# Kernel optimization log

Hardware: AMD Instinct MI355X
Metric: run time of the kernel (lower is better)

Reference implementation:

```python
import jax, jax.numpy as jnp
import numpy as np

SELECT_SIZE = 64
SM_SCALE = 0.07216878364870322  # 192 ** -0.5
V_HEAD_DIM = 128


def setup_inputs() -> dict:
    key = jax.random.key(0)
    k1, k2, k3, k4 = jax.random.split(key, 4)
    B, S, Hq, G, TOPK = 4, 2048, 16, 4, 16
    T = B * S
    NB = S // SELECT_SIZE  # 32 blocks per sequence
    q = jax.random.normal(k1, (T, Hq, 192), dtype=jnp.float32)
    k = jax.random.normal(k2, (T, Hq, 192), dtype=jnp.float32)
    v = jax.random.normal(k3, (T, Hq, V_HEAD_DIM), dtype=jnp.float32)
    idx = jax.random.randint(k4, (T, G, TOPK), 0, NB, dtype=jnp.int32)
    # guarantee block 0 is always selected so every causal row has >=1 valid key
    idx = idx.at[..., 0].set(0)
    idx = jnp.sort(idx, axis=-1)
    return {"q": q, "k": k, "v": v, "selected_indices": idx,
            "batch_size": B, "seq_len": S}


def reference(q, k, v, selected_indices, batch_size, seq_len):
    B, S = batch_size, seq_len
    Hq = q.shape[1]
    G = selected_indices.shape[1]
    Hg = Hq // G  # query heads per selection-score group
    nb = (S + SELECT_SIZE - 1) // SELECT_SIZE
    dv = v.shape[-1]

    # un-ragged: B equal-length sequences
    qg = q.reshape(B, S, G, Hg, -1)
    kg = k.reshape(B, S, G, Hg, -1)
    vg = v.reshape(B, S, G, Hg, -1)
    idx = selected_indices.reshape(B, S, G, -1)

    # which KV blocks are selected for each (query position, group): [B,S,G,nb]
    allowed_blk = (idx[..., None] == jnp.arange(nb, dtype=idx.dtype)).any(axis=-2)
    blk_of_pos = jnp.arange(S) // SELECT_SIZE
    pos_ok = allowed_blk[..., blk_of_pos]  # [B, Tq, G, Skv]
    causal = jnp.arange(S)[:, None] >= jnp.arange(S)[None, :]
    mask = pos_ok & causal[None, :, None, :]          # [B, Tq, G, Skv]
    mask = mask.transpose(0, 2, 1, 3)[:, :, None]      # [B, G, 1, Tq, Skv]

    scores = jnp.einsum('btghd,bsghd->bghts', qg, kg) * SM_SCALE
    scores = jnp.where(mask, scores, jnp.float32(-1e30))
    attn = jax.nn.softmax(scores, axis=-1)
    o = jnp.einsum('bghts,bsghd->btghd', attn, vg)
    return o.reshape(B * S, Hq * dv)
```

## Files before the change

### kernel.cpp

```cpp
#include <hip/hip_runtime.h>


typedef __attribute__((ext_vector_type(8))) _Float16 half8;
typedef __attribute__((ext_vector_type(4))) float f32x4;
typedef __attribute__((ext_vector_type(4))) unsigned int u32x4;

__device__ __forceinline__ half8 cvt8(const float4* p) {
  float4 a = p[0], b = p[1];
  half8 r;
  r[0] = (_Float16)a.x; r[1] = (_Float16)a.y; r[2] = (_Float16)a.z; r[3] = (_Float16)a.w;
  r[4] = (_Float16)b.x; r[5] = (_Float16)b.y; r[6] = (_Float16)b.z; r[7] = (_Float16)b.w;
  return r;
}

__device__ __forceinline__ half8 cvt8s(const float4* p, float s) {
  float4 a = p[0], b = p[1];
  half8 r;
  r[0] = (_Float16)(a.x * s); r[1] = (_Float16)(a.y * s);
  r[2] = (_Float16)(a.z * s); r[3] = (_Float16)(a.w * s);
  r[4] = (_Float16)(b.x * s); r[5] = (_Float16)(b.y * s);
  r[6] = (_Float16)(b.z * s); r[7] = (_Float16)(b.w * s);
  return r;
}

__device__ __forceinline__ void async16(const void* g, void* l) {
  __builtin_amdgcn_global_load_lds(
      (const __attribute__((address_space(1))) void*)g,
      (__attribute__((address_space(3))) void*)l, 16, 0, 0);
}

__device__ __forceinline__ f32x4 vmax4(f32x4 a, f32x4 b) {
  f32x4 r;
  r[0] = fmaxf(a[0], b[0]); r[1] = fmaxf(a[1], b[1]);
  r[2] = fmaxf(a[2], b[2]); r[3] = fmaxf(a[3], b[3]);
  return r;
}

__global__ __launch_bounds__(256) void kv_prep(const float* __restrict__ k,
                                               const float* __restrict__ v,
                                               _Float16* __restrict__ kf,
                                               _Float16* __restrict__ vf) {
  __shared__ float lb[64 * 196];
  int blk = blockIdx.x;
  int bh = blk >> 5, kb = blk & 31;
  int b = bh >> 4, h = bh & 15;
  int tid = threadIdx.x;

  const float* ksrc = k + ((long)(b * 2048 + kb * 64) * 16 + h) * 192;
#pragma unroll
  for (int it = 0; it < 12; ++it) {
    int idx = it * 256 + tid;
    int kk = idx / 48, c4 = idx - kk * 48;
    *(float4*)(&lb[kk * 196 + c4 * 4]) = *(const float4*)(ksrc + (long)kk * 3072 + c4 * 4);
  }
  __syncthreads();
  _Float16* kdst = kf + (long)blk * 12288;
#pragma unroll
  for (int it = 0; it < 6; ++it) {
    int oct = it * 256 + tid;
    int frag = oct >> 6, lane = oct & 63;
    int ntile = frag / 6, kc = frag - ntile * 6;
    int lm = lane & 15;
    int n = ((lm >> 2) << 4) + ntile * 4 + (lm & 3);
    int d = kc * 32 + ((lane >> 4) << 3);
    *(half8*)(kdst + (long)oct * 8) = cvt8((const float4*)(&lb[n * 196 + d]));
  }
  __syncthreads();

  const float* vsrc = v + ((long)(b * 2048 + kb * 64) * 16 + h) * 128;
#pragma unroll
  for (int it = 0; it < 8; ++it) {
    int idx = it * 256 + tid;
    int kk = idx >> 5, c4 = idx & 31;
    *(float4*)(&lb[kk * 132 + c4 * 4]) = *(const float4*)(vsrc + (long)kk * 2048 + c4 * 4);
  }
  __syncthreads();
  _Float16* vdst = vf + (long)blk * 8192;
#pragma unroll
  for (int it = 0; it < 4; ++it) {
    int oct = it * 256 + tid;
    int frag = oct >> 6, lane = oct & 63;
    int n0 = frag >> 1, kc = frag & 1;
    int dv = n0 * 16 + (lane & 15);
    int kbase = kc * 32 + ((lane >> 4) << 3);
    half8 o;
#pragma unroll
    for (int j = 0; j < 8; ++j) o[j] = (_Float16)lb[(kbase + j) * 132 + dv];
    *(half8*)(vdst + (long)oct * 8) = o;
  }
}

__global__ __launch_bounds__(256) void attn_main(const float* __restrict__ q,
                                                 const int* __restrict__ idx,
                                                 const _Float16* __restrict__ kf,
                                                 const _Float16* __restrict__ vf,
                                                 float* __restrict__ out) {
  constexpr float SCL = 0.07216878364870322f * 1.4426950408889634f;
  int id = (int)blockIdx.x;
  int qb = 31 - (id >> 6);
  int h = id & 15, b = (id >> 4) & 3, g = h >> 2;
  int tid = threadIdx.x;
  int w = tid >> 6, L = tid & 63;
  int Lm = L & 15, Lq = L >> 4;
  int m0 = w * 16;
  int t0 = b * 2048 + qb * 64;

  __shared__ __align__(16) char sh_kv[40960];
  __shared__ __align__(16) _Float16 Pbuf[4][16 * 72];
  __shared__ unsigned un_sh[4];
  char* lk = sh_kv;
  char* lv = sh_kv + 24576;

  half8 qa[6];
  const float* qrow = q + ((long)(t0 + m0 + Lm) * 16 + h) * 192;
#pragma unroll
  for (int c = 0; c < 6; ++c) qa[c] = cvt8s((const float4*)(qrow + c * 32 + Lq * 8), SCL);

  unsigned mrow = 0;
  {
    const int* ip = idx + ((long)(t0 + m0 + Lm) * 4 + g) * 16;
#pragma unroll
    for (int j = 0; j < 16; ++j) mrow |= (1u << ip[j]);
  }
  unsigned un = mrow;
#pragma unroll
  for (int o = 32; o; o >>= 1) un |= __shfl_xor(un, o, 64);
  if (L == 0) un_sh[w] = un;
  __syncthreads();
  unsigned bm = un_sh[0] | un_sh[1] | un_sh[2] | un_sh[3];

  f32x4 Oacc[8];
#pragma unroll
  for (int n0 = 0; n0 < 8; ++n0) Oacc[n0] = (f32x4){0.f, 0.f, 0.f, 0.f};
  float m_i = -1e30f, l_i = 0.f;

  const char* kfb = (const char*)(kf + (long)((b * 16 + h) * 32) * 12288);
  const char* vfb = (const char*)(vf + (long)((b * 16 + h) * 32) * 8192);
  _Float16* pw = &Pbuf[w][0];
  const half8* lkf = (const half8*)lk;
  const half8* lvf = (const half8*)lv;

  auto stage = [&](int kb) {
    const char* kg = kfb + (long)kb * 24576;
    const char* vg = vfb + (long)kb * 16384;
#pragma unroll
    for (int c = 0; c < 6; ++c) {
      int ch = w + c * 4;
      async16(kg + ch * 1024 + L * 16, lk + ch * 1024);
    }
#pragma unroll
    for (int c = 0; c < 4; ++c) {
      int ch = w + c * 4;
      async16(vg + ch * 1024 + L * 16, lv + ch * 1024);
    }
  };

  auto compute = [&](int kb, bool lastb) __attribute__((always_inline)) {
    f32x4 S[4];
#pragma unroll
    for (int nt = 0; nt < 4; ++nt) {
      f32x4 acc = {0.f, 0.f, 0.f, 0.f};
#pragma unroll
      for (int c = 0; c < 6; ++c)
        acc = __builtin_amdgcn_mfma_f32_16x16x32_f16(lkf[(nt * 6 + c) * 64 + L], qa[c], acc, 0, 0, 0);
      S[nt] = acc;
    }

    float p[4][4];
    float msel = ((mrow >> kb) & 1u) ? 1.0f : 0.0f;
    if (!lastb) {
      f32x4 t = vmax4(vmax4(S[0], S[1]), vmax4(S[2], S[3]));
      float rmax = fmaxf(fmaxf(t[0], t[1]), fmaxf(t[2], t[3]));
      rmax = fmaxf(rmax, __shfl_xor(rmax, 16));
      rmax = fmaxf(rmax, __shfl_xor(rmax, 32));
      if (__any(rmax > m_i)) {
        float mn = fmaxf(m_i, rmax);
        float av = __builtin_amdgcn_exp2f(m_i - mn);
        m_i = mn;
        l_i *= av;
#pragma unroll
        for (int n0 = 0; n0 < 8; ++n0) Oacc[n0] *= av;
      }
      float ps[4];
#pragma unroll
      for (int nt = 0; nt < 4; ++nt) {
        float s0 = 0.f, s1 = 0.f;
#pragma unroll
        for (int i = 0; i < 4; i += 2) {
          float a = __builtin_amdgcn_exp2f(S[nt][i] - m_i) * msel;
          float c = __builtin_amdgcn_exp2f(S[nt][i + 1] - m_i) * msel;
          p[nt][i] = a; p[nt][i + 1] = c;
          s0 += a; s1 += c;
        }
        ps[nt] = s0 + s1;
      }
      float psum = (ps[0] + ps[1]) + (ps[2] + ps[3]);
      psum += __shfl_xor(psum, 16);
      psum += __shfl_xor(psum, 32);
      l_i += psum;
    } else {
      float sc[4][4];
      float rmax = -1e30f;
#pragma unroll
      for (int nt = 0; nt < 4; ++nt)
#pragma unroll
        for (int i = 0; i < 4; ++i) {
          int key = Lq * 16 + nt * 4 + i;
          bool ok = (msel != 0.f) && (key <= m0 + Lm);
          float v = ok ? S[nt][i] : -1e30f;
          sc[nt][i] = v;
          rmax = fmaxf(rmax, v);
        }
      rmax = fmaxf(rmax, __shfl_xor(rmax, 16));
      rmax = fmaxf(rmax, __shfl_xor(rmax, 32));
      float mn = fmaxf(m_i, rmax);
      float av = __builtin_amdgcn_exp2f(m_i - mn);
      m_i = mn;
      float ps[4];
#pragma unroll
      for (int nt = 0; nt < 4; ++nt) {
        float s0 = 0.f;
#pragma unroll
        for (int i = 0; i < 4; ++i) {
          float a = __builtin_amdgcn_exp2f(sc[nt][i] - mn);
          p[nt][i] = a;
          s0 += a;
        }
        ps[nt] = s0;
      }
      float psum = (ps[0] + ps[1]) + (ps[2] + ps[3]);
      psum += __shfl_xor(psum, 16);
      psum += __shfl_xor(psum, 32);
      l_i = l_i * av + psum;
#pragma unroll
      for (int n0 = 0; n0 < 8; ++n0) Oacc[n0] *= av;
    }

    asm volatile("s_waitcnt lgkmcnt(0)" ::: "memory");
    u32x4 w0, w1;
    {
      auto c00 = __builtin_amdgcn_cvt_pkrtz(p[0][0], p[0][1]);
      auto c01 = __builtin_amdgcn_cvt_pkrtz(p[0][2], p[0][3]);
      auto c10 = __builtin_amdgcn_cvt_pkrtz(p[1][0], p[1][1]);
      auto c11 = __builtin_amdgcn_cvt_pkrtz(p[1][2], p[1][3]);
      auto c20 = __builtin_amdgcn_cvt_pkrtz(p[2][0], p[2][1]);
      auto c21 = __builtin_amdgcn_cvt_pkrtz(p[2][2], p[2][3]);
      auto c30 = __builtin_amdgcn_cvt_pkrtz(p[3][0], p[3][1]);
      auto c31 = __builtin_amdgcn_cvt_pkrtz(p[3][2], p[3][3]);
      w0[0] = __builtin_bit_cast(unsigned, c00); w0[1] = __builtin_bit_cast(unsigned, c01);
      w0[2] = __builtin_bit_cast(unsigned, c10); w0[3] = __builtin_bit_cast(unsigned, c11);
      w1[0] = __builtin_bit_cast(unsigned, c20); w1[1] = __builtin_bit_cast(unsigned, c21);
      w1[2] = __builtin_bit_cast(unsigned, c30); w1[3] = __builtin_bit_cast(unsigned, c31);
    }
    *(u32x4*)(pw + Lm * 72 + Lq * 16) = w0;
    *(u32x4*)(pw + Lm * 72 + Lq * 16 + 8) = w1;
    asm volatile("s_waitcnt lgkmcnt(0)" ::: "memory");

#pragma unroll
    for (int kc = 0; kc < 2; ++kc) {
      half8 pfr = *(const half8*)(pw + Lm * 72 + kc * 32 + Lq * 8);
#pragma unroll
      for (int n0 = 0; n0 < 8; ++n0)
        Oacc[n0] = __builtin_amdgcn_mfma_f32_16x16x32_f16(lvf[(n0 * 2 + kc) * 64 + L], pfr, Oacc[n0], 0, 0, 0);
    }
  };

  for (int kb = 0; kb < qb; ++kb) {
    if (!((bm >> kb) & 1u)) continue;
    stage(kb);
    asm volatile("s_waitcnt vmcnt(0)" ::: "memory");
    __syncthreads();
    if ((un >> kb) & 1u) compute(kb, false);
    __syncthreads();
  }
  if ((bm >> qb) & 1u) {
    stage(qb);
    asm volatile("s_waitcnt vmcnt(0)" ::: "memory");
    __syncthreads();
    if ((un >> qb) & 1u) compute(qb, true);
  }

  float inv = 1.f / l_i;
  float* orow = out + (long)(t0 + m0 + Lm) * 2048 + h * 128 + Lq * 4;
#pragma unroll
  for (int n0 = 0; n0 < 8; ++n0) {
    f32x4 o = Oacc[n0] * inv;
    *(f32x4*)(orow + n0 * 16) = o;
  }
}

extern "C" void kernel_launch(void* const* d_in, const int* in_sizes, int n_in,
                              void* d_out, int out_size, void* d_ws, size_t ws_size,
                              hipStream_t stream) {
  const float* q = (const float*)d_in[0];
  const float* k = (const float*)d_in[1];
  const float* v = (const float*)d_in[2];
  const int* idx = (const int*)d_in[3];
  _Float16* kf = (_Float16*)d_ws;
  _Float16* vf = kf + (size_t)2048 * 12288;
  float* out = (float*)d_out;
  kv_prep<<<2048, 256, 0, stream>>>(k, v, kf, vf);
  attn_main<<<2048, 256, 0, stream>>>(q, idx, kf, vf, out);
}
```

Baseline: 404.8 us.

## Double-buffer K in LDS, prefetch V into registers, iterate selected blocks by bitmask

Replaces the load-wait-compute loop over a single shared K/V buffer with a software pipeline. K now sits in two LDS buffers, and the next selected block is staged while the current one is computed. V is read straight into registers, one set per wave, instead of going through LDS. The loop walks set bits of the selected-block mask, each iteration ends with a partial vmcnt wait plus barrier, and the idx bitmask build is vectorized with shuffles. The aim is to hide global load latency and cut the syncs per block, at the cost of more VGPRs, four-fold redundant V global reads per workgroup, and computing blocks that some waves do not need.

```diff
diff --git a/kernel.cpp b/kernel.cpp
--- a/kernel.cpp
+++ b/kernel.cpp
@@ -105,57 +105,73 @@
   int m0 = w * 16;
   int t0 = b * 2048 + qb * 64;
 
-  __shared__ __align__(16) char sh_kv[40960];
+  __shared__ __align__(16) char sh_k[2][24576];
   __shared__ __align__(16) _Float16 Pbuf[4][16 * 72];
   __shared__ unsigned un_sh[4];
-  char* lk = sh_kv;
-  char* lv = sh_kv + 24576;
+
+  const char* kfb = (const char*)(kf + (long)((b * 16 + h) * 32) * 12288);
+  const _Float16* vfb = vf + (long)((b * 16 + h) * 32) * 8192;
+  _Float16* pw = &Pbuf[w][0];
+
+  auto stageK = [&](int kb, char* dst) {
+    const char* kg = kfb + (long)kb * 24576;
+#pragma unroll
+    for (int c = 0; c < 6; ++c) {
+      int ch = w + c * 4;
+      async16(kg + ch * 1024 + L * 16, dst + ch * 1024);
+    }
+  };
+
+  half8 vr[16];
+  auto loadV = [&](int kb) {
+    const half8* vg = (const half8*)(vfb + (long)kb * 8192);
+#pragma unroll
+    for (int j = 0; j < 16; ++j) vr[j] = vg[j * 64 + L];
+  };
 
   half8 qa[6];
   const float* qrow = q + ((long)(t0 + m0 + Lm) * 16 + h) * 192;
 #pragma unroll
   for (int c = 0; c < 6; ++c) qa[c] = cvt8s((const float4*)(qrow + c * 32 + Lq * 8), SCL);
 
-  unsigned mrow = 0;
+  stageK(0, sh_k[0]);
+  loadV(0);
+
+  unsigned mrow;
   {
-    const int* ip = idx + ((long)(t0 + m0 + Lm) * 4 + g) * 16;
-#pragma unroll
-    for (int j = 0; j < 16; ++j) mrow |= (1u << ip[j]);
+    const int4* ip = (const int4*)(idx + ((long)(t0 + m0 + Lm) * 4 + g) * 16);
+    int4 iv = ip[Lq];
+    unsigned mr = (1u << iv.x) | (1u << iv.y) | (1u << iv.z) | (1u << iv.w);
+    mr |= __shfl_xor(mr, 16);
+    mr |= __shfl_xor(mr, 32);
+    mrow = mr;
   }
   unsigned un = mrow;
-#pragma unroll
-  for (int o = 32; o; o >>= 1) un |= __shfl_xor(un, o, 64);
+  un |= __shfl_xor(un, 1);
+  un |= __shfl_xor(un, 2);
+  un |= __shfl_xor(un, 4);
+  un |= __shfl_xor(un, 8);
   if (L == 0) un_sh[w] = un;
   __syncthreads();
   unsigned bm = un_sh[0] | un_sh[1] | un_sh[2] | un_sh[3];
+  unsigned bmask = bm & ((2u << qb) - 1);
 
   f32x4 Oacc[8];
 #pragma unroll
   for (int n0 = 0; n0 < 8; ++n0) Oacc[n0] = (f32x4){0.f, 0.f, 0.f, 0.f};
   float m_i = -1e30f, l_i = 0.f;
 
-  const char* kfb = (const char*)(kf + (long)((b * 16 + h) * 32) * 12288);
-  const char* vfb = (const char*)(vf + (long)((b * 16 + h) * 32) * 8192);
-  _Float16* pw = &Pbuf[w][0];
-  const half8* lkf = (const half8*)lk;
-  const half8* lvf = (const half8*)lv;
-
-  auto stage = [&](int kb) {
-    const char* kg = kfb + (long)kb * 24576;
-    const char* vg = vfb + (long)kb * 16384;
-#pragma unroll
-    for (int c = 0; c < 6; ++c) {
-      int ch = w + c * 4;
-      async16(kg + ch * 1024 + L * 16, lk + ch * 1024);
-    }
-#pragma unroll
-    for (int c = 0; c < 4; ++c) {
-      int ch = w + c * 4;
-      async16(vg + ch * 1024 + L * 16, lv + ch * 1024);
-    }
-  };
-
-  auto compute = [&](int kb, bool lastb) __attribute__((always_inline)) {
+  unsigned rem = bmask;
+  int kb = 0;
+  int cur = 0;
+
+  for (;;) {
+    rem &= rem - 1;
+    int nxt = rem ? (int)__builtin_ctz(rem) : -1;
+    if (nxt >= 0) stageK(nxt, sh_k[cur ^ 1]);
+
+    const half8* lkf = (const half8*)sh_k[cur];
+
     f32x4 S[4];
 #pragma unroll
     for (int nt = 0; nt < 4; ++nt) {
@@ -168,7 +184,7 @@
 
     float p[4][4];
     float msel = ((mrow >> kb) & 1u) ? 1.0f : 0.0f;
-    if (!lastb) {
+    if (kb != qb) {
       f32x4 t = vmax4(vmax4(S[0], S[1]), vmax4(S[2], S[3]));
       float rmax = fmaxf(fmaxf(t[0], t[1]), fmaxf(t[2], t[3]));
       rmax = fmaxf(rmax, __shfl_xor(rmax, 16));
@@ -261,23 +277,14 @@
       half8 pfr = *(const half8*)(pw + Lm * 72 + kc * 32 + Lq * 8);
 #pragma unroll
       for (int n0 = 0; n0 < 8; ++n0)
-        Oacc[n0] = __builtin_amdgcn_mfma_f32_16x16x32_f16(lvf[(n0 * 2 + kc) * 64 + L], pfr, Oacc[n0], 0, 0, 0);
-    }
-  };
-
-  for (int kb = 0; kb < qb; ++kb) {
-    if (!((bm >> kb) & 1u)) continue;
-    stage(kb);
-    asm volatile("s_waitcnt vmcnt(0)" ::: "memory");
-    __syncthreads();
-    if ((un >> kb) & 1u) compute(kb, false);
-    __syncthreads();
-  }
-  if ((bm >> qb) & 1u) {
-    stage(qb);
-    asm volatile("s_waitcnt vmcnt(0)" ::: "memory");
-    __syncthreads();
-    if ((un >> qb) & 1u) compute(qb, true);
+        Oacc[n0] = __builtin_amdgcn_mfma_f32_16x16x32_f16(vr[n0 * 2 + kc], pfr, Oacc[n0], 0, 0, 0);
+    }
+
+    if (nxt < 0) break;
+    loadV(nxt);
+    asm volatile("s_waitcnt vmcnt(16)\n\ts_barrier" ::: "memory");
+    cur ^= 1;
+    kb = nxt;
   }
 
   float inv = 1.f / l_i;
```

After: 439.7 us. 1.09x slower.
